# Optimization experiments

Measured on AMD Instinct MI355X. Metric: run time of the kernel, lower is better.

## Reference

```python
import jax, jax.numpy as jnp
import numpy as np

N_NODES = 100000
N_EDGES = 6400000


def setup_inputs() -> dict:
    key = jax.random.key(0)
    ks = jax.random.split(key, 20)
    g = lambda i, shape, fan_in: jax.random.normal(ks[i], shape, dtype=jnp.float32) / np.sqrt(fan_in)
    inp = {
        "x": jax.random.normal(ks[0], (N_NODES, 32), dtype=jnp.float32),
        "edge_index": jax.random.randint(ks[1], (2, N_EDGES), 0, N_NODES, dtype=jnp.int64),
        # encoder: Linear(32,240) -> ReLU -> Linear(240,24) -> ReLU
        "enc_w1": g(2, (32, 240), 32), "enc_b1": jnp.zeros((240,), jnp.float32),
        "enc_w2": g(3, (240, 24), 240), "enc_b2": jnp.zeros((24,), jnp.float32),
        # lin_r (applied to root, no bias) -- PyG defaults
        "sage1_wl": g(4, (24, 24), 24), "sage1_bl": jnp.zeros((24,), jnp.float32), "sage1_wr": g(5, (24, 24), 24),
        "sage2_wl": g(6, (24, 24), 24), "sage2_bl": jnp.zeros((24,), jnp.float32), "sage2_wr": g(7, (24, 24), 24),
        "sage3_wl": g(8, (24, 24), 24), "sage3_bl": jnp.zeros((24,), jnp.float32), "sage3_wr": g(9, (24, 24), 24),
        # decoder: Linear(24,120) -> ReLU -> Linear(120,12)
        "dec_w1": g(10, (24, 120), 24), "dec_b1": jnp.zeros((120,), jnp.float32),
        "dec_w2": g(11, (120, 12), 120), "dec_b2": jnp.zeros((12,), jnp.float32),
    }
    return inp


def _sage_conv(x, src, dst, wl, bl, wr, n_nodes):
    # mean aggregation: gather source features, scatter-sum at targets, divide by degree
    msg = x[src]                                                   # [E, H]
    agg = jax.ops.segment_sum(msg, dst, num_segments=n_nodes)      # [N, H]
    deg = jax.ops.segment_sum(jnp.ones((src.shape[0],), x.dtype), dst, num_segments=n_nodes)
    mean = agg / jnp.maximum(deg, 1.0)[:, None]
    return mean @ wl + bl + x @ wr


def reference(x, edge_index, enc_w1, enc_b1, enc_w2, enc_b2,
              sage1_wl, sage1_bl, sage1_wr,
              sage2_wl, sage2_bl, sage2_wr,
              sage3_wl, sage3_bl, sage3_wr,
              dec_w1, dec_b1, dec_w2, dec_b2):
    n = x.shape[0]
    src, dst = edge_index[0], edge_index[1]
    # encoder
    h = jax.nn.relu(x @ enc_w1 + enc_b1)
    h = jax.nn.relu(h @ enc_w2 + enc_b2)
    # GNN: SAGEConv -> ReLU -> SAGEConv -> ReLU -> SAGEConv
    h = jax.nn.relu(_sage_conv(h, src, dst, sage1_wl, sage1_bl, sage1_wr, n))
    h = jax.nn.relu(_sage_conv(h, src, dst, sage2_wl, sage2_bl, sage2_wr, n))
    h = _sage_conv(h, src, dst, sage3_wl, sage3_bl, sage3_wr, n)
    # decoder
    h = jax.nn.relu(h @ dec_w1 + dec_b1)
    return h @ dec_w2 + dec_b2
```

## Files before the change

### kernel.cpp

```cpp
#include <hip/hip_runtime.h>
#include <hip/hip_bf16.h>

#define N_NODES 100000
#define N_EDGES 6400000
#define BROW 24
#define PROW 8
#define BUCKET_SIZE 256
#define N_BUCKETS ((N_NODES + BUCKET_SIZE - 1) / BUCKET_SIZE)
#define BUCKET_CAP 17920
#define STAGE_CAP 26624
#define SENT 0xFFFFFFFFu
#define STAGE_BLOCKS 1024
#define CHUNK (N_EDGES / STAGE_BLOCKS)
#define TOTAL_A (STAGE_BLOCKS + 2 * N_BUCKETS)

typedef float floatx2 __attribute__((ext_vector_type(2)));

__device__ __forceinline__ unsigned short f2bf(float f) {
    unsigned u = __float_as_uint(f);
    unsigned r = (u + 0x7fffu + ((u >> 16) & 1u)) >> 16;
    return (unsigned short)r;
}

__device__ __forceinline__ unsigned pack_fp8_4(float a, float b, float c, float d) {
    int w = __builtin_amdgcn_cvt_pk_fp8_f32(a, b, 0, false);
    w = __builtin_amdgcn_cvt_pk_fp8_f32(c, d, w, true);
    return (unsigned)w;
}

#define DEC4(w, arr, j) { \
    floatx2 lo_ = __builtin_amdgcn_cvt_pk_f32_fp8((int)(w), false); \
    floatx2 hi_ = __builtin_amdgcn_cvt_pk_f32_fp8((int)(w), true);  \
    arr[j] += lo_.x; arr[(j)+1] += lo_.y; arr[(j)+2] += hi_.x; arr[(j)+3] += hi_.y; }

#define SET2(u, arr, j) { arr[j] = __uint_as_float((u) << 16); arr[(j)+1] = __uint_as_float((u) & 0xffff0000u); }
#define ADD2(u, arr, j) { arr[j] += __uint_as_float((u) << 16); arr[(j)+1] += __uint_as_float((u) & 0xffff0000u); }

#define GATHER1(sidx, acc) { \
    const uint4* rp_ = (const uint4*)(Ptab + (size_t)(sidx) * PROW); \
    uint4 A_ = rp_[0]; \
    uint2 B_ = ((const uint2*)rp_)[2]; \
    DEC4(A_.x, acc, 0)  DEC4(A_.y, acc, 4)  DEC4(A_.z, acc, 8) \
    DEC4(A_.w, acc,12)  DEC4(B_.x, acc,16)  DEC4(B_.y, acc,20) }

__global__ __launch_bounds__(256) void k_transpose_w1(
    const float* __restrict__ w1, float* __restrict__ w1t)
{
    int tid = blockIdx.x * blockDim.x + threadIdx.x;
    if (tid < 32 * 240) {
        int k = tid >> 5, i = tid & 31;
        w1t[tid] = w1[i * 240 + k];
    }
}

__global__ __launch_bounds__(256) void k_stage_enc(
    const int* __restrict__ src, const int* __restrict__ dst,
    int* __restrict__ cursor, unsigned* __restrict__ stage,
    const float* __restrict__ x,
    const float* __restrict__ w1t, const float* __restrict__ b1,
    const float* __restrict__ w2,
    unsigned short* __restrict__ pb0, unsigned short* __restrict__ pb1)
{
    __shared__ int cnt[N_BUCKETS];
    __shared__ int bse[N_BUCKETS];
    __shared__ int lof[N_BUCKETS];
    __shared__ int cur[N_BUCKETS];
    __shared__ int ps[512];
    __shared__ unsigned sbuf[CHUNK];
    int t = threadIdx.x;

    long long ii = blockIdx.x;
    int a0 = (int)((ii * STAGE_BLOCKS) / TOTAL_A);
    int a1 = (int)(((ii + 1) * STAGE_BLOCKS) / TOTAL_A);

    if (a1 > a0) {
        int e0 = a0 * CHUNK;
        int e1 = min(e0 + CHUNK, N_EDGES);

        for (int i = t; i < N_BUCKETS; i += 256) cnt[i] = 0;
        __syncthreads();
        for (int e = e0 + t; e < e1; e += 256)
            atomicAdd(&cnt[dst[e] >> 8], 1);
        __syncthreads();
        for (int i = t; i < N_BUCKETS; i += 256) {
            int c = cnt[i];
            int c16 = (c + 15) & ~15;
            bse[i] = c16 ? atomicAdd(&cursor[i * 16], c16) : 0;
            cur[i] = 0;
        }
        ps[t]       = (t < N_BUCKETS) ? cnt[t] : 0;
        ps[t + 256] = (t + 256 < N_BUCKETS) ? cnt[t + 256] : 0;
        __syncthreads();
        for (int off = 1; off < 512; off <<= 1) {
            int a  = (t >= off) ? ps[t - off] : 0;
            int b2 = (t + 256 >= off) ? ps[t + 256 - off] : 0;
            __syncthreads();
            ps[t] += a;
            ps[t + 256] += b2;
            __syncthreads();
        }
        for (int i = t; i < N_BUCKETS; i += 256) lof[i] = ps[i] - cnt[i];
        __syncthreads();
        for (int e = e0 + t; e < e1; e += 256) {
            int d = dst[e];
            int s = src[e];
            int b = d >> 8;
            int pos = atomicAdd(&cur[b], 1);
            sbuf[lof[b] + pos] = ((unsigned)(d & 255) << 17) | (unsigned)s;
        }
        __syncthreads();
        int wid = t >> 6, lane = t & 63;
        for (int b = wid; b < N_BUCKETS; b += 4) {
            int c = cnt[b];
            int c16 = (c + 15) & ~15;
            unsigned* gp = stage + (size_t)b * STAGE_CAP + bse[b];
            const unsigned* lp = sbuf + lof[b];
            for (int j = lane; j < c16; j += 64)
                gp[j] = (j < c) ? lp[j] : SENT;
        }
    } else {
        int eb = (int)(ii - a0);
        int nb = eb >> 1;
        int chunk = eb & 1;
        int n = nb * 256 + t;
        if (n >= N_NODES) return;

        float xr[32];
        const float4* xv = (const float4*)(x + (size_t)n * 32);
#pragma unroll
        for (int i = 0; i < 8; ++i) {
            float4 v = xv[i];
            xr[4*i+0] = v.x; xr[4*i+1] = v.y; xr[4*i+2] = v.z; xr[4*i+3] = v.w;
        }
        float acc[24];
#pragma unroll
        for (int j = 0; j < 24; ++j) acc[j] = 0.f;

        int k0 = chunk * 120;
        for (int k = k0; k < k0 + 120; ++k) {
            const float4* wr = (const float4*)(w1t + k * 32);
            float tt = b1[k];
#pragma unroll
            for (int q = 0; q < 8; ++q) {
                float4 w = wr[q];
                tt += xr[4*q+0] * w.x + xr[4*q+1] * w.y + xr[4*q+2] * w.z + xr[4*q+3] * w.w;
            }
            tt = fmaxf(tt, 0.f);
            const float* w2r = w2 + k * 24;
#pragma unroll
            for (int j = 0; j < 24; ++j) acc[j] += tt * w2r[j];
        }
        unsigned wb[12];
#pragma unroll
        for (int j = 0; j < 24; ++j) {
            if (j & 1) wb[j >> 1] |= (unsigned)f2bf(acc[j]) << 16;
            else       wb[j >> 1]  = (unsigned)f2bf(acc[j]);
        }
        unsigned short* pb = chunk ? pb1 : pb0;
        uint4* ob = (uint4*)(pb + (size_t)n * BROW);
#pragma unroll
        for (int q = 0; q < 3; ++q)
            ob[q] = make_uint4(wb[4*q], wb[4*q+1], wb[4*q+2], wb[4*q+3]);
    }
}

__global__ __launch_bounds__(256) void k_fill_encxf(
    const unsigned* __restrict__ stage, const int* __restrict__ cursor,
    int* __restrict__ csr, int* __restrict__ deg,
    float* __restrict__ recip, int* __restrict__ row_ptr,
    const unsigned short* __restrict__ pb0, const unsigned short* __restrict__ pb1,
    const float* __restrict__ b2,
    const float* __restrict__ wl, const float* __restrict__ wr,
    unsigned* __restrict__ Ptab, float* __restrict__ Qtab)
{
    __shared__ int dl[BUCKET_SIZE];
    __shared__ int s[BUCKET_SIZE];
    __shared__ int fcur[BUCKET_SIZE];
    int t = threadIdx.x;

    if (blockIdx.x < N_BUCKETS) {
        int b = blockIdx.x;
        int ne = cursor[b * 16];
        const unsigned* sp = stage + (size_t)b * STAGE_CAP;

        dl[t] = 0;
        __syncthreads();
        for (int i = t; i < ne; i += 256) {
            unsigned v = sp[i];
            if (v != SENT) atomicAdd(&dl[v >> 17], 1);
        }
        __syncthreads();
        int d = dl[t];
        int d4 = (d + 3) & ~3;
        s[t] = d4;
        __syncthreads();
        for (int off = 1; off < 256; off <<= 1) {
            int v = (t >= off) ? s[t - off] : 0;
            __syncthreads();
            s[t] += v;
            __syncthreads();
        }
        int excl = s[t] - d4;
        fcur[t] = excl;
        int n = b * BUCKET_SIZE + t;
        if (n < N_NODES) {
            deg[n] = d;
            recip[n] = 1.0f / (float)max(d, 1);
            row_ptr[n] = b * BUCKET_CAP + excl;
        }
        __syncthreads();
        int* cb = csr + (size_t)b * BUCKET_CAP;
        for (int i = t; i < ne; i += 256) {
            unsigned v = sp[i];
            if (v == SENT) continue;
            int slot = atomicAdd(&fcur[v >> 17], 1);
            cb[slot] = (int)(v & 0x1FFFFu);
        }
        __syncthreads();
        if (n < N_NODES) {
            for (int j = d; j < d4; ++j) cb[excl + j] = N_NODES;
        }
    } else {
        int n = (blockIdx.x - N_BUCKETS) * 256 + t;
        if (n >= N_NODES) return;
        float h[24];
        {
            const uint4* hp = (const uint4*)(pb0 + (size_t)n * BROW);
            uint4 A = hp[0], B = hp[1], C = hp[2];
            SET2(A.x, h, 0)  SET2(A.y, h, 2)  SET2(A.z, h, 4)  SET2(A.w, h, 6)
            SET2(B.x, h, 8)  SET2(B.y, h,10)  SET2(B.z, h,12)  SET2(B.w, h,14)
            SET2(C.x, h,16)  SET2(C.y, h,18)  SET2(C.z, h,20)  SET2(C.w, h,22)
        }
        {
            const uint4* hp = (const uint4*)(pb1 + (size_t)n * BROW);
            uint4 A = hp[0], B = hp[1], C = hp[2];
            ADD2(A.x, h, 0)  ADD2(A.y, h, 2)  ADD2(A.z, h, 4)  ADD2(A.w, h, 6)
            ADD2(B.x, h, 8)  ADD2(B.y, h,10)  ADD2(B.z, h,12)  ADD2(B.w, h,14)
            ADD2(C.x, h,16)  ADD2(C.y, h,18)  ADD2(C.z, h,20)  ADD2(C.w, h,22)
        }
#pragma unroll
        for (int j = 0; j < 24; ++j) h[j] = fmaxf(h[j] + b2[j], 0.f);

        float p[24], q[24];
#pragma unroll
        for (int j = 0; j < 24; ++j) { p[j] = 0.f; q[j] = 0.f; }
#pragma unroll
        for (int k = 0; k < 24; ++k) {
            float hk = h[k];
#pragma unroll
            for (int j = 0; j < 24; ++j) {
                p[j] += hk * wl[k * 24 + j];
                q[j] += hk * wr[k * 24 + j];
            }
        }
        unsigned w8[6];
#pragma unroll
        for (int c = 0; c < 6; ++c)
            w8[c] = pack_fp8_4(p[4*c], p[4*c+1], p[4*c+2], p[4*c+3]);
        uint4* ob = (uint4*)(Ptab + (size_t)n * PROW);
        ob[0] = make_uint4(w8[0], w8[1], w8[2], w8[3]);
        ob[1] = make_uint4(w8[4], w8[5], 0u, 0u);
        float4* qb = (float4*)(Qtab + (size_t)n * 24);
#pragma unroll
        for (int c = 0; c < 6; ++c)
            qb[c] = make_float4(q[4*c], q[4*c+1], q[4*c+2], q[4*c+3]);
        if (n == 0) {
            uint4* zb = (uint4*)(Ptab + (size_t)N_NODES * PROW);
            zb[0] = make_uint4(0u,0u,0u,0u);
            zb[1] = make_uint4(0u,0u,0u,0u);
        }
    }
}

__global__ __launch_bounds__(256) void k_xform(
    const unsigned short* __restrict__ hin,
    const float* __restrict__ wl, const float* __restrict__ wr,
    unsigned* __restrict__ Ptab, float* __restrict__ Qtab)
{
    int n = blockIdx.x * blockDim.x + threadIdx.x;
    if (n >= N_NODES) return;
    float h[24];
    {
        const uint4* hp = (const uint4*)(hin + (size_t)n * BROW);
        uint4 A = hp[0], B = hp[1], C = hp[2];
        SET2(A.x, h, 0)  SET2(A.y, h, 2)  SET2(A.z, h, 4)  SET2(A.w, h, 6)
        SET2(B.x, h, 8)  SET2(B.y, h,10)  SET2(B.z, h,12)  SET2(B.w, h,14)
        SET2(C.x, h,16)  SET2(C.y, h,18)  SET2(C.z, h,20)  SET2(C.w, h,22)
    }
    float p[24], q[24];
#pragma unroll
    for (int j = 0; j < 24; ++j) { p[j] = 0.f; q[j] = 0.f; }
#pragma unroll
    for (int k = 0; k < 24; ++k) {
        float hk = h[k];
#pragma unroll
        for (int j = 0; j < 24; ++j) {
            p[j] += hk * wl[k * 24 + j];
            q[j] += hk * wr[k * 24 + j];
        }
    }
    unsigned w8[6];
#pragma unroll
    for (int c = 0; c < 6; ++c)
        w8[c] = pack_fp8_4(p[4*c], p[4*c+1], p[4*c+2], p[4*c+3]);
    uint4* ob = (uint4*)(Ptab + (size_t)n * PROW);
    ob[0] = make_uint4(w8[0], w8[1], w8[2], w8[3]);
    ob[1] = make_uint4(w8[4], w8[5], 0u, 0u);
    float4* qb = (float4*)(Qtab + (size_t)n * 24);
#pragma unroll
    for (int c = 0; c < 6; ++c)
        qb[c] = make_float4(q[4*c], q[4*c+1], q[4*c+2], q[4*c+3]);
    if (n == 0) {
        uint4* zb = (uint4*)(Ptab + (size_t)N_NODES * PROW);
        zb[0] = make_uint4(0u,0u,0u,0u);
        zb[1] = make_uint4(0u,0u,0u,0u);
    }
}

template <bool RELU>
__global__ __launch_bounds__(256, 4) void k_agg(
    const unsigned* __restrict__ Ptab, const float* __restrict__ Qtab,
    const int* __restrict__ row_ptr, const int* __restrict__ deg,
    const float* __restrict__ recip, const int* __restrict__ csr,
    const float* __restrict__ bl,
    unsigned short* __restrict__ houtb)
{
    int gt = blockIdx.x * blockDim.x + threadIdx.x;
    int n = gt >> 3, g = gt & 7;
    if (n >= N_NODES) return;
    int start = row_ptr[n];
    int cnt4 = (deg[n] + 3) & ~3;

    float acc[24];
#pragma unroll
    for (int j = 0; j < 24; ++j) acc[j] = 0.f;

    for (int i0 = 4 * g; i0 < cnt4; i0 += 32) {
        int4 s4 = *(const int4*)(csr + start + i0);
        GATHER1(s4.x, acc)
        GATHER1(s4.y, acc)
        GATHER1(s4.z, acc)
        GATHER1(s4.w, acc)
    }
#pragma unroll
    for (int m = 1; m <= 4; m <<= 1)
#pragma unroll
        for (int j = 0; j < 24; ++j) acc[j] += __shfl_xor(acc[j], m, 64);

    if (g < 3) {
        float rc = recip[n];
        const float4* qb = (const float4*)(Qtab + (size_t)n * 24 + g * 8);
        float4 q0 = qb[0], q1 = qb[1];
        float qv[8] = {q0.x, q0.y, q0.z, q0.w, q1.x, q1.y, q1.z, q1.w};
        unsigned wb[4];
#pragma unroll
        for (int jj = 0; jj < 8; ++jj) {
            int j = g * 8 + jj;
            float v = acc[j] * rc + qv[jj] + bl[j];
            if (RELU) v = fmaxf(v, 0.f);
            if (jj & 1) wb[jj >> 1] |= (unsigned)f2bf(v) << 16;
            else        wb[jj >> 1]  = (unsigned)f2bf(v);
        }
        ((uint4*)(houtb + (size_t)n * BROW))[g] = make_uint4(wb[0], wb[1], wb[2], wb[3]);
    }
}

__global__ __launch_bounds__(256, 4) void k_agg3(
    const unsigned* __restrict__ Ptab, const float* __restrict__ Qtab,
    const int* __restrict__ row_ptr, const int* __restrict__ deg,
    const float* __restrict__ recip, const int* __restrict__ csr,
    const float* __restrict__ bl,
    float* __restrict__ o3)
{
    int gt = blockIdx.x * blockDim.x + threadIdx.x;
    int n = gt >> 3, g = gt & 7;
    if (n >= N_NODES) return;
    int start = row_ptr[n];
    int cnt4 = (deg[n] + 3) & ~3;

    float acc[24];
#pragma unroll
    for (int j = 0; j < 24; ++j) acc[j] = 0.f;

    for (int i0 = 4 * g; i0 < cnt4; i0 += 32) {
        int4 s4 = *(const int4*)(csr + start + i0);
        GATHER1(s4.x, acc)
        GATHER1(s4.y, acc)
        GATHER1(s4.z, acc)
        GATHER1(s4.w, acc)
    }
#pragma unroll
    for (int m = 1; m <= 4; m <<= 1)
#pragma unroll
        for (int j = 0; j < 24; ++j) acc[j] += __shfl_xor(acc[j], m, 64);

    if (g < 3) {
        float rc = recip[n];
        const float4* qb = (const float4*)(Qtab + (size_t)n * 24 + g * 8);
        float4 q0 = qb[0], q1 = qb[1];
        float qv[8] = {q0.x, q0.y, q0.z, q0.w, q1.x, q1.y, q1.z, q1.w};
        float ov[8];
#pragma unroll
        for (int jj = 0; jj < 8; ++jj)
            ov[jj] = acc[g * 8 + jj] * rc + qv[jj] + bl[g * 8 + jj];
        float4* op = (float4*)(o3 + (size_t)n * 24 + g * 8);
        op[0] = make_float4(ov[0], ov[1], ov[2], ov[3]);
        op[1] = make_float4(ov[4], ov[5], ov[6], ov[7]);
    }
}

__global__ __launch_bounds__(256) void k_decoder(
    const float* __restrict__ o3,
    const float* __restrict__ w1, const float* __restrict__ b1,
    const float* __restrict__ w2, const float* __restrict__ b2,
    float* __restrict__ out)
{
    int n = blockIdx.x * blockDim.x + threadIdx.x;
    if (n >= N_NODES) return;
    float h[24];
    const float4* hv = (const float4*)(o3 + (size_t)n * 24);
#pragma unroll
    for (int q = 0; q < 6; ++q) {
        float4 v = hv[q];
        h[4*q+0] = v.x; h[4*q+1] = v.y; h[4*q+2] = v.z; h[4*q+3] = v.w;
    }
    float acc[12];
#pragma unroll
    for (int j = 0; j < 12; ++j) acc[j] = b2[j];
    for (int k = 0; k < 120; ++k) {
        float t = b1[k];
#pragma unroll
        for (int i = 0; i < 24; ++i) t += h[i] * w1[i * 120 + k];
        t = fmaxf(t, 0.f);
#pragma unroll
        for (int j = 0; j < 12; ++j) acc[j] += t * w2[k * 12 + j];
    }
    float* o = out + (size_t)n * 12;
#pragma unroll
    for (int j = 0; j < 12; ++j) o[j] = acc[j];
}

static inline size_t align_up(size_t v, size_t a) { return (v + a - 1) & ~(a - 1); }

extern "C" void kernel_launch(void* const* d_in, const int* in_sizes, int n_in,
                              void* d_out, int out_size, void* d_ws, size_t ws_size,
                              hipStream_t stream)
{
    (void)in_sizes; (void)n_in; (void)out_size; (void)ws_size;

    const float* x    = (const float*)d_in[0];
    const int*  edge  = (const int*)d_in[1];
    const int*  esrc  = edge;
    const int*  edst  = edge + N_EDGES;
    const float* enc_w1 = (const float*)d_in[2];
    const float* enc_b1 = (const float*)d_in[3];
    const float* enc_w2 = (const float*)d_in[4];
    const float* enc_b2 = (const float*)d_in[5];
    const float* s1_wl = (const float*)d_in[6];
    const float* s1_bl = (const float*)d_in[7];
    const float* s1_wr = (const float*)d_in[8];
    const float* s2_wl = (const float*)d_in[9];
    const float* s2_bl = (const float*)d_in[10];
    const float* s2_wr = (const float*)d_in[11];
    const float* s3_wl = (const float*)d_in[12];
    const float* s3_bl = (const float*)d_in[13];
    const float* s3_wr = (const float*)d_in[14];
    const float* dec_w1 = (const float*)d_in[15];
    const float* dec_b1 = (const float*)d_in[16];
    const float* dec_w2 = (const float*)d_in[17];
    const float* dec_b2 = (const float*)d_in[18];
    float* out = (float*)d_out;

    char* base = (char*)d_ws;
    size_t off = 0;
    auto carve = [&](size_t bytes) { size_t o = off; off = align_up(off + bytes, 256); return (void*)(base + o); };
    char* stage_region = (char*)carve((size_t)N_BUCKETS * STAGE_CAP * sizeof(unsigned));
    unsigned* stage = (unsigned*)stage_region;
    float* o3       = (float*)stage_region;
    int*   csr      = (int*)carve((size_t)N_BUCKETS * BUCKET_CAP * sizeof(int));
    unsigned* Ptab  = (unsigned*)carve((size_t)(N_NODES + 1) * PROW * sizeof(unsigned));
    float* Qtab     = (float*)carve((size_t)N_NODES * 24 * sizeof(float));
    unsigned short* h0b = (unsigned short*)carve((size_t)N_NODES * BROW * sizeof(unsigned short));
    unsigned short* h1b = (unsigned short*)carve((size_t)N_NODES * BROW * sizeof(unsigned short));
    int*   deg     = (int*)  carve((size_t)N_NODES * sizeof(int));
    float* recip   = (float*)carve((size_t)N_NODES * sizeof(float));
    int*   row_ptr = (int*)  carve((size_t)N_NODES * sizeof(int));
    int*   cursor  = (int*)  carve((size_t)N_BUCKETS * 16 * sizeof(int));
    float* w1t     = (float*)carve((size_t)240 * 32 * sizeof(float));

    const int NB_N = (N_NODES + 255) / 256;
    const int NB8  = (N_NODES * 8 + 255) / 256;

    hipMemsetAsync(cursor, 0, (size_t)N_BUCKETS * 16 * sizeof(int), stream);
    k_transpose_w1<<<30, 256, 0, stream>>>(enc_w1, w1t);

    k_stage_enc<<<TOTAL_A, 256, 0, stream>>>(
        esrc, edst, cursor, stage, x, w1t, enc_b1, enc_w2, h0b, h1b);

    k_fill_encxf<<<NB_N * 2, 256, 0, stream>>>(
        stage, cursor, csr, deg, recip, row_ptr,
        h0b, h1b, enc_b2, s1_wl, s1_wr, Ptab, Qtab);

    k_agg<true><<<NB8, 256, 0, stream>>>(Ptab, Qtab, row_ptr, deg, recip, csr, s1_bl, h1b);
    k_xform<<<NB_N, 256, 0, stream>>>(h1b, s2_wl, s2_wr, Ptab, Qtab);
    k_agg<true><<<NB8, 256, 0, stream>>>(Ptab, Qtab, row_ptr, deg, recip, csr, s2_bl, h0b);
    k_xform<<<NB_N, 256, 0, stream>>>(h0b, s3_wl, s3_wr, Ptab, Qtab);
    k_agg3<<<NB8, 256, 0, stream>>>(Ptab, Qtab, row_ptr, deg, recip, csr, s3_bl, o3);
    k_decoder<<<NB_N, 256, 0, stream>>>(o3, dec_w1, dec_b1, dec_w2, dec_b2, out);
}
```

Measured before the change: 507.4 us.

## Move encoder MLP from staging kernel into fill kernel, halve stage blocks

Encoder MLP work is moved out of the edge-bucketing stage kernel and co-scheduled with the CSR fill kernel. The encoder finalize plus first-layer transform becomes its own kernel. Staging now uses 512 blocks with larger chunks (more LDS per block) and a smaller per-bucket stage capacity, which cuts per-bucket padding and cursor atomics. The goal is better balance of the compute-heavy encoder against memory-bound passes, at the cost of one extra launch and lower occupancy in staging.

```diff
diff --git a/kernel.cpp b/kernel.cpp
--- a/kernel.cpp
+++ b/kernel.cpp
@@ -8,11 +8,10 @@
 #define BUCKET_SIZE 256
 #define N_BUCKETS ((N_NODES + BUCKET_SIZE - 1) / BUCKET_SIZE)
 #define BUCKET_CAP 17920
-#define STAGE_CAP 26624
+#define STAGE_CAP 22528
 #define SENT 0xFFFFFFFFu
-#define STAGE_BLOCKS 1024
-#define CHUNK (N_EDGES / STAGE_BLOCKS)
-#define TOTAL_A (STAGE_BLOCKS + 2 * N_BUCKETS)
+#define STAGE_BLOCKS 512
+#define CHUNK ((N_EDGES + STAGE_BLOCKS - 1) / STAGE_BLOCKS)
 
 typedef float floatx2 __attribute__((ext_vector_type(2)));
 
@@ -53,13 +52,9 @@
     }
 }
 
-__global__ __launch_bounds__(256) void k_stage_enc(
+__global__ __launch_bounds__(256) void k_stage1(
     const int* __restrict__ src, const int* __restrict__ dst,
-    int* __restrict__ cursor, unsigned* __restrict__ stage,
-    const float* __restrict__ x,
-    const float* __restrict__ w1t, const float* __restrict__ b1,
-    const float* __restrict__ w2,
-    unsigned short* __restrict__ pb0, unsigned short* __restrict__ pb1)
+    int* __restrict__ cursor, unsigned* __restrict__ stage)
 {
     __shared__ int cnt[N_BUCKETS];
     __shared__ int bse[N_BUCKETS];
@@ -68,110 +63,60 @@
     __shared__ int ps[512];
     __shared__ unsigned sbuf[CHUNK];
     int t = threadIdx.x;
-
-    long long ii = blockIdx.x;
-    int a0 = (int)((ii * STAGE_BLOCKS) / TOTAL_A);
-    int a1 = (int)(((ii + 1) * STAGE_BLOCKS) / TOTAL_A);
-
-    if (a1 > a0) {
-        int e0 = a0 * CHUNK;
-        int e1 = min(e0 + CHUNK, N_EDGES);
-
-        for (int i = t; i < N_BUCKETS; i += 256) cnt[i] = 0;
-        __syncthreads();
-        for (int e = e0 + t; e < e1; e += 256)
-            atomicAdd(&cnt[dst[e] >> 8], 1);
-        __syncthreads();
-        for (int i = t; i < N_BUCKETS; i += 256) {
-            int c = cnt[i];
-            int c16 = (c + 15) & ~15;
-            bse[i] = c16 ? atomicAdd(&cursor[i * 16], c16) : 0;
-            cur[i] = 0;
-        }
-        ps[t]       = (t < N_BUCKETS) ? cnt[t] : 0;
-        ps[t + 256] = (t + 256 < N_BUCKETS) ? cnt[t + 256] : 0;
-        __syncthreads();
-        for (int off = 1; off < 512; off <<= 1) {
-            int a  = (t >= off) ? ps[t - off] : 0;
-            int b2 = (t + 256 >= off) ? ps[t + 256 - off] : 0;
-            __syncthreads();
-            ps[t] += a;
-            ps[t + 256] += b2;
-            __syncthreads();
-        }
-        for (int i = t; i < N_BUCKETS; i += 256) lof[i] = ps[i] - cnt[i];
-        __syncthreads();
-        for (int e = e0 + t; e < e1; e += 256) {
-            int d = dst[e];
-            int s = src[e];
-            int b = d >> 8;
-            int pos = atomicAdd(&cur[b], 1);
-            sbuf[lof[b] + pos] = ((unsigned)(d & 255) << 17) | (unsigned)s;
-        }
-        __syncthreads();
-        int wid = t >> 6, lane = t & 63;
-        for (int b = wid; b < N_BUCKETS; b += 4) {
-            int c = cnt[b];
-            int c16 = (c + 15) & ~15;
-            unsigned* gp = stage + (size_t)b * STAGE_CAP + bse[b];
-            const unsigned* lp = sbuf + lof[b];
-            for (int j = lane; j < c16; j += 64)
-                gp[j] = (j < c) ? lp[j] : SENT;
-        }
-    } else {
-        int eb = (int)(ii - a0);
-        int nb = eb >> 1;
-        int chunk = eb & 1;
-        int n = nb * 256 + t;
-        if (n >= N_NODES) return;
-
-        float xr[32];
-        const float4* xv = (const float4*)(x + (size_t)n * 32);
-#pragma unroll
-        for (int i = 0; i < 8; ++i) {
-            float4 v = xv[i];
-            xr[4*i+0] = v.x; xr[4*i+1] = v.y; xr[4*i+2] = v.z; xr[4*i+3] = v.w;
-        }
-        float acc[24];
-#pragma unroll
-        for (int j = 0; j < 24; ++j) acc[j] = 0.f;
-
-        int k0 = chunk * 120;
-        for (int k = k0; k < k0 + 120; ++k) {
-            const float4* wr = (const float4*)(w1t + k * 32);
-            float tt = b1[k];
-#pragma unroll
-            for (int q = 0; q < 8; ++q) {
-                float4 w = wr[q];
-                tt += xr[4*q+0] * w.x + xr[4*q+1] * w.y + xr[4*q+2] * w.z + xr[4*q+3] * w.w;
-            }
-            tt = fmaxf(tt, 0.f);
-            const float* w2r = w2 + k * 24;
-#pragma unroll
-            for (int j = 0; j < 24; ++j) acc[j] += tt * w2r[j];
-        }
-        unsigned wb[12];
-#pragma unroll
-        for (int j = 0; j < 24; ++j) {
-            if (j & 1) wb[j >> 1] |= (unsigned)f2bf(acc[j]) << 16;
-            else       wb[j >> 1]  = (unsigned)f2bf(acc[j]);
-        }
-        unsigned short* pb = chunk ? pb1 : pb0;
-        uint4* ob = (uint4*)(pb + (size_t)n * BROW);
-#pragma unroll
-        for (int q = 0; q < 3; ++q)
-            ob[q] = make_uint4(wb[4*q], wb[4*q+1], wb[4*q+2], wb[4*q+3]);
-    }
-}
-
-__global__ __launch_bounds__(256) void k_fill_encxf(
+    int e0 = blockIdx.x * CHUNK;
+    int e1 = min(e0 + CHUNK, N_EDGES);
+
+    for (int i = t; i < N_BUCKETS; i += 256) cnt[i] = 0;
+    __syncthreads();
+    for (int e = e0 + t; e < e1; e += 256)
+        atomicAdd(&cnt[dst[e] >> 8], 1);
+    __syncthreads();
+    for (int i = t; i < N_BUCKETS; i += 256) {
+        int c = cnt[i];
+        int c16 = (c + 15) & ~15;
+        bse[i] = c16 ? atomicAdd(&cursor[i * 16], c16) : 0;
+        cur[i] = 0;
+    }
+    ps[t]       = (t < N_BUCKETS) ? cnt[t] : 0;
+    ps[t + 256] = (t + 256 < N_BUCKETS) ? cnt[t + 256] : 0;
+    __syncthreads();
+    for (int off = 1; off < 512; off <<= 1) {
+        int a  = (t >= off) ? ps[t - off] : 0;
+        int b2 = (t + 256 >= off) ? ps[t + 256 - off] : 0;
+        __syncthreads();
+        ps[t] += a;
+        ps[t + 256] += b2;
+        __syncthreads();
+    }
+    for (int i = t; i < N_BUCKETS; i += 256) lof[i] = ps[i] - cnt[i];
+    __syncthreads();
+    for (int e = e0 + t; e < e1; e += 256) {
+        int d = dst[e];
+        int s = src[e];
+        int b = d >> 8;
+        int pos = atomicAdd(&cur[b], 1);
+        sbuf[lof[b] + pos] = ((unsigned)(d & 255) << 17) | (unsigned)s;
+    }
+    __syncthreads();
+    int wid = t >> 6, lane = t & 63;
+    for (int b = wid; b < N_BUCKETS; b += 4) {
+        int c = cnt[b];
+        int c16 = (c + 15) & ~15;
+        unsigned* gp = stage + (size_t)b * STAGE_CAP + bse[b];
+        const unsigned* lp = sbuf + lof[b];
+        for (int j = lane; j < c16; j += 64)
+            gp[j] = (j < c) ? lp[j] : SENT;
+    }
+}
+
+__global__ __launch_bounds__(256) void k_fill_enc(
     const unsigned* __restrict__ stage, const int* __restrict__ cursor,
     int* __restrict__ csr, int* __restrict__ deg,
     float* __restrict__ recip, int* __restrict__ row_ptr,
-    const unsigned short* __restrict__ pb0, const unsigned short* __restrict__ pb1,
-    const float* __restrict__ b2,
-    const float* __restrict__ wl, const float* __restrict__ wr,
-    unsigned* __restrict__ Ptab, float* __restrict__ Qtab)
+    const float* __restrict__ x,
+    const float* __restrict__ w1t, const float* __restrict__ b1,
+    const float* __restrict__ w2,
+    unsigned short* __restrict__ pb0, unsigned short* __restrict__ pb1)
 {
     __shared__ int dl[BUCKET_SIZE];
     __shared__ int s[BUCKET_SIZE];
@@ -221,54 +166,104 @@
             for (int j = d; j < d4; ++j) cb[excl + j] = N_NODES;
         }
     } else {
-        int n = (blockIdx.x - N_BUCKETS) * 256 + t;
+        int bid = blockIdx.x - N_BUCKETS;
+        int nb = bid >> 1;
+        int chunk = bid & 1;
+        int n = nb * 256 + t;
         if (n >= N_NODES) return;
-        float h[24];
-        {
-            const uint4* hp = (const uint4*)(pb0 + (size_t)n * BROW);
-            uint4 A = hp[0], B = hp[1], C = hp[2];
-            SET2(A.x, h, 0)  SET2(A.y, h, 2)  SET2(A.z, h, 4)  SET2(A.w, h, 6)
-            SET2(B.x, h, 8)  SET2(B.y, h,10)  SET2(B.z, h,12)  SET2(B.w, h,14)
-            SET2(C.x, h,16)  SET2(C.y, h,18)  SET2(C.z, h,20)  SET2(C.w, h,22)
-        }
-        {
-            const uint4* hp = (const uint4*)(pb1 + (size_t)n * BROW);
-            uint4 A = hp[0], B = hp[1], C = hp[2];
-            ADD2(A.x, h, 0)  ADD2(A.y, h, 2)  ADD2(A.z, h, 4)  ADD2(A.w, h, 6)
-            ADD2(B.x, h, 8)  ADD2(B.y, h,10)  ADD2(B.z, h,12)  ADD2(B.w, h,14)
-            ADD2(C.x, h,16)  ADD2(C.y, h,18)  ADD2(C.z, h,20)  ADD2(C.w, h,22)
-        }
-#pragma unroll
-        for (int j = 0; j < 24; ++j) h[j] = fmaxf(h[j] + b2[j], 0.f);
-
-        float p[24], q[24];
-#pragma unroll
-        for (int j = 0; j < 24; ++j) { p[j] = 0.f; q[j] = 0.f; }
-#pragma unroll
-        for (int k = 0; k < 24; ++k) {
-            float hk = h[k];
-#pragma unroll
-            for (int j = 0; j < 24; ++j) {
-                p[j] += hk * wl[k * 24 + j];
-                q[j] += hk * wr[k * 24 + j];
+
+        float xr[32];
+        const float4* xv = (const float4*)(x + (size_t)n * 32);
+#pragma unroll
+        for (int i = 0; i < 8; ++i) {
+            float4 v = xv[i];
+            xr[4*i+0] = v.x; xr[4*i+1] = v.y; xr[4*i+2] = v.z; xr[4*i+3] = v.w;
+        }
+        float acc[24];
+#pragma unroll
+        for (int j = 0; j < 24; ++j) acc[j] = 0.f;
+
+        int k0 = chunk * 120;
+        for (int k = k0; k < k0 + 120; ++k) {
+            const float4* wr = (const float4*)(w1t + k * 32);
+            float tt = b1[k];
+#pragma unroll
+            for (int q = 0; q < 8; ++q) {
+                float4 w = wr[q];
+                tt += xr[4*q+0] * w.x + xr[4*q+1] * w.y + xr[4*q+2] * w.z + xr[4*q+3] * w.w;
             }
-        }
-        unsigned w8[6];
-#pragma unroll
-        for (int c = 0; c < 6; ++c)
-            w8[c] = pack_fp8_4(p[4*c], p[4*c+1], p[4*c+2], p[4*c+3]);
-        uint4* ob = (uint4*)(Ptab + (size_t)n * PROW);
-        ob[0] = make_uint4(w8[0], w8[1], w8[2], w8[3]);
-        ob[1] = make_uint4(w8[4], w8[5], 0u, 0u);
-        float4* qb = (float4*)(Qtab + (size_t)n * 24);
-#pragma unroll
-        for (int c = 0; c < 6; ++c)
-            qb[c] = make_float4(q[4*c], q[4*c+1], q[4*c+2], q[4*c+3]);
-        if (n == 0) {
-            uint4* zb = (uint4*)(Ptab + (size_t)N_NODES * PROW);
-            zb[0] = make_uint4(0u,0u,0u,0u);
-            zb[1] = make_uint4(0u,0u,0u,0u);
-        }
+            tt = fmaxf(tt, 0.f);
+            const float* w2r = w2 + k * 24;
+#pragma unroll
+            for (int j = 0; j < 24; ++j) acc[j] += tt * w2r[j];
+        }
+        unsigned wb[12];
+#pragma unroll
+        for (int j = 0; j < 24; ++j) {
+            if (j & 1) wb[j >> 1] |= (unsigned)f2bf(acc[j]) << 16;
+            else       wb[j >> 1]  = (unsigned)f2bf(acc[j]);
+        }
+        unsigned short* pb = chunk ? pb1 : pb0;
+        uint4* ob = (uint4*)(pb + (size_t)n * BROW);
+#pragma unroll
+        for (int q = 0; q < 3; ++q)
+            ob[q] = make_uint4(wb[4*q], wb[4*q+1], wb[4*q+2], wb[4*q+3]);
+    }
+}
+
+__global__ __launch_bounds__(256) void k_encfin_xform(
+    const unsigned short* __restrict__ pb0, const unsigned short* __restrict__ pb1,
+    const float* __restrict__ b2,
+    const float* __restrict__ wl, const float* __restrict__ wr,
+    unsigned* __restrict__ Ptab, float* __restrict__ Qtab)
+{
+    int n = blockIdx.x * blockDim.x + threadIdx.x;
+    if (n >= N_NODES) return;
+    float h[24];
+    {
+        const uint4* hp = (const uint4*)(pb0 + (size_t)n * BROW);
+        uint4 A = hp[0], B = hp[1], C = hp[2];
+        SET2(A.x, h, 0)  SET2(A.y, h, 2)  SET2(A.z, h, 4)  SET2(A.w, h, 6)
+        SET2(B.x, h, 8)  SET2(B.y, h,10)  SET2(B.z, h,12)  SET2(B.w, h,14)
+        SET2(C.x, h,16)  SET2(C.y, h,18)  SET2(C.z, h,20)  SET2(C.w, h,22)
+    }
+    {
+        const uint4* hp = (const uint4*)(pb1 + (size_t)n * BROW);
+        uint4 A = hp[0], B = hp[1], C = hp[2];
+        ADD2(A.x, h, 0)  ADD2(A.y, h, 2)  ADD2(A.z, h, 4)  ADD2(A.w, h, 6)
+        ADD2(B.x, h, 8)  ADD2(B.y, h,10)  ADD2(B.z, h,12)  ADD2(B.w, h,14)
+        ADD2(C.x, h,16)  ADD2(C.y, h,18)  ADD2(C.z, h,20)  ADD2(C.w, h,22)
+    }
+#pragma unroll
+    for (int j = 0; j < 24; ++j) h[j] = fmaxf(h[j] + b2[j], 0.f);
+
+    float p[24], q[24];
+#pragma unroll
+    for (int j = 0; j < 24; ++j) { p[j] = 0.f; q[j] = 0.f; }
+#pragma unroll
+    for (int k = 0; k < 24; ++k) {
+        float hk = h[k];
+#pragma unroll
+        for (int j = 0; j < 24; ++j) {
+            p[j] += hk * wl[k * 24 + j];
+            q[j] += hk * wr[k * 24 + j];
+        }
+    }
+    unsigned w8[6];
+#pragma unroll
+    for (int c = 0; c < 6; ++c)
+        w8[c] = pack_fp8_4(p[4*c], p[4*c+1], p[4*c+2], p[4*c+3]);
+    uint4* ob = (uint4*)(Ptab + (size_t)n * PROW);
+    ob[0] = make_uint4(w8[0], w8[1], w8[2], w8[3]);
+    ob[1] = make_uint4(w8[4], w8[5], 0u, 0u);
+    float4* qb = (float4*)(Qtab + (size_t)n * 24);
+#pragma unroll
+    for (int c = 0; c < 6; ++c)
+        qb[c] = make_float4(q[4*c], q[4*c+1], q[4*c+2], q[4*c+3]);
+    if (n == 0) {
+        uint4* zb = (uint4*)(Ptab + (size_t)N_NODES * PROW);
+        zb[0] = make_uint4(0u,0u,0u,0u);
+        zb[1] = make_uint4(0u,0u,0u,0u);
     }
 }
 
@@ -493,14 +488,13 @@
 
     hipMemsetAsync(cursor, 0, (size_t)N_BUCKETS * 16 * sizeof(int), stream);
     k_transpose_w1<<<30, 256, 0, stream>>>(enc_w1, w1t);
-
-    k_stage_enc<<<TOTAL_A, 256, 0, stream>>>(
-        esrc, edst, cursor, stage, x, w1t, enc_b1, enc_w2, h0b, h1b);
-
-    k_fill_encxf<<<NB_N * 2, 256, 0, stream>>>(
+    k_stage1<<<STAGE_BLOCKS, 256, 0, stream>>>(esrc, edst, cursor, stage);
+
+    k_fill_enc<<<NB_N * 3, 256, 0, stream>>>(
         stage, cursor, csr, deg, recip, row_ptr,
-        h0b, h1b, enc_b2, s1_wl, s1_wr, Ptab, Qtab);
-
+        x, w1t, enc_b1, enc_w2, h0b, h1b);
+
+    k_encfin_xform<<<NB_N, 256, 0, stream>>>(h0b, h1b, enc_b2, s1_wl, s1_wr, Ptab, Qtab);
     k_agg<true><<<NB8, 256, 0, stream>>>(Ptab, Qtab, row_ptr, deg, recip, csr, s1_bl, h1b);
     k_xform<<<NB_N, 256, 0, stream>>>(h1b, s2_wl, s2_wr, Ptab, Qtab);
     k_agg<true><<<NB8, 256, 0, stream>>>(Ptab, Qtab, row_ptr, deg, recip, csr, s2_bl, h0b);
```

New measurement: 477.0 us. 1.06x faster.
